# Optimization experiments

Measured on AMD Instinct MI355X. Metric: run time of the kernel, lower is better.

The kernel has to match this reference:

```python
import jax, jax.numpy as jnp
import numpy as np

N = 100000
E = 800000
D_IN = 128
D_HID = 128
D_EMB = 128
D_OUT = 2


def setup_inputs() -> dict:
    key = jax.random.key(0)
    ks = jax.random.split(key, 16)
    x = jax.random.normal(ks[0], (N, D_IN), dtype=jnp.float32)
    edge_index = jax.random.randint(ks[1], (2, E), 0, N, dtype=jnp.int64)

    def lin(k, d_out, d_in, scale):
        return jax.random.normal(k, (d_out, d_in), dtype=jnp.float32) * scale

    s1 = 1.0 / np.sqrt(D_IN)
    s2 = 1.0 / np.sqrt(D_HID)
    s3 = 1.0 / np.sqrt(D_EMB)
    return {
        "x": x,
        "edge_index": edge_index,
        # layer 1: in -> hidden  (lin_l has bias, lin_r no bias, as in PyG SAGEConv)
        "Wl1": lin(ks[2], D_HID, D_IN, s1), "bl1": jnp.zeros((D_HID,), jnp.float32),
        "Wr1": lin(ks[3], D_HID, D_IN, s1),
        # layer 2: hidden -> hidden
        "Wl2": lin(ks[4], D_HID, D_HID, s2), "bl2": jnp.zeros((D_HID,), jnp.float32),
        "Wr2": lin(ks[5], D_HID, D_HID, s2),
        # layer 3: hidden -> embedding
        "Wl3": lin(ks[6], D_EMB, D_HID, s2), "bl3": jnp.zeros((D_EMB,), jnp.float32),
        "Wr3": lin(ks[7], D_EMB, D_HID, s2),
        # output head: embedding -> output (bias)
        "Wo": lin(ks[8], D_OUT, D_EMB, s3), "bo": jnp.zeros((D_OUT,), jnp.float32),
    }


def _sage_conv(x, src, dst, Wl, bl, Wr):
    # mean-aggregate neighbor (source) features onto destination nodes
    msg = x[src]                                             # [E, d]
    agg = jax.ops.segment_sum(msg, dst, num_segments=N)      # [N, d]
    deg = jax.ops.segment_sum(jnp.ones((src.shape[0],), x.dtype), dst, num_segments=N)
    agg = agg / jnp.maximum(deg, 1.0)[:, None]
    # out = lin_l(agg) + lin_r(x)
    return agg @ Wl.T + bl + x @ Wr.T


def reference(x, edge_index, Wl1, bl1, Wr1, Wl2, bl2, Wr2, Wl3, bl3, Wr3, Wo, bo):
    src, dst = edge_index[0], edge_index[1]
    h = jax.nn.relu(_sage_conv(x, src, dst, Wl1, bl1, Wr1))   # dropout is identity in eval
    h = jax.nn.relu(_sage_conv(h, src, dst, Wl2, bl2, Wr2))
    h = _sage_conv(h, src, dst, Wl3, bl3, Wr3)                # no relu on last conv
    return h @ Wo.T + bo                                      # [N, D_OUT]
```

## Files before the change

### kernel.cpp

```cpp
#include <hip/hip_runtime.h>
#include <stdint.h>

typedef unsigned int u32;
typedef unsigned short u16;
typedef __bf16 bf16x8 __attribute__((ext_vector_type(8)));
typedef float floatx16 __attribute__((ext_vector_type(16)));
typedef u32 u32x4 __attribute__((ext_vector_type(4)));
typedef float floatx4 __attribute__((ext_vector_type(4)));

__device__ __forceinline__ u16 f2b(float f) {
    u32 u = __builtin_bit_cast(u32, f);
    u32 r = u + 0x7FFFu + ((u >> 16) & 1u);
    return (u16)(r >> 16);
}
__device__ __forceinline__ float lo2f(u32 u) { return __builtin_bit_cast(float, u << 16); }
__device__ __forceinline__ float hi2f(u32 u) { return __builtin_bit_cast(float, u & 0xFFFF0000u); }

__device__ __forceinline__ void self_detect(const int* ei, const u32* xw, int& is64, int& isbf) {
    int lane = threadIdx.x & 63;
    int v = ei ? ei[2 * lane + 1] : 0;
    unsigned long long b1 = __ballot(v == 0);
    u32 w = xw ? xw[lane] : 0;
    u32 e = (w >> 7) & 0xFF;
    int plaus = (e == 0) || (e >= 90 && e <= 140);
    unsigned long long b2 = __ballot(plaus);
    is64 = (b1 == ~0ULL) ? 1 : 0;
    isbf = (b2 == ~0ULL) ? 1 : 0;
}

__device__ __forceinline__ int load_id(const int* __restrict__ ei, int is64, size_t pos, int N) {
    int v = is64 ? ei[2 * pos] : ei[pos];
    unsigned u = (unsigned)v;
    if (u >= (unsigned)N) u = 0;
    return (int)u;
}

__device__ __forceinline__ float load_f(const void* __restrict__ p, int isbf, size_t i) {
    if (isbf) {
        u16 s = ((const u16*)p)[i];
        return __builtin_bit_cast(float, ((u32)s) << 16);
    }
    return ((const float*)p)[i];
}

#define CH 4096
#define CAPB 3072

__global__ __launch_bounds__(1024) void front_kernel(
    const void* __restrict__ xraw, const int* __restrict__ ei, int E, int N, int cvb,
    u32* __restrict__ xb, int* __restrict__ gcur, u32* __restrict__ csrbkt,
    const void* Wl1, const void* Wr1, const void* Wl2, const void* Wr2,
    const void* Wl3, const void* Wr3, const void* b1, const void* b2,
    const void* b3, const void* Wo, const void* bo,
    u16* __restrict__ Wcp, float* __restrict__ smalls) {
    __shared__ int lhist[1024], loff[1024], lcur[1024], gofs[1024], wsum[16];
    __shared__ u32 ebuf[CH];
    __shared__ u16 ebkt[CH];
    int blk = blockIdx.x;
    int t = threadIdx.x;

    if (blk < cvb) {
        int is64, isbf;
        self_detect(nullptr, (const u32*)xraw, is64, isbf);
        int i = blk * 1024 + t;
        int count4 = N * 16;
        if (i >= count4) return;
        if (isbf) {
            ((u32x4*)xb)[i] = ((const u32x4*)xraw)[i];
        } else {
            const floatx4* f4 = (const floatx4*)xraw;
            floatx4 f0 = f4[2 * i], f1 = f4[2 * i + 1];
            u32x4 o;
            o.x = (u32)f2b(f0.x) | ((u32)f2b(f0.y) << 16);
            o.y = (u32)f2b(f0.z) | ((u32)f2b(f0.w) << 16);
            o.z = (u32)f2b(f1.x) | ((u32)f2b(f1.y) << 16);
            o.w = (u32)f2b(f1.z) | ((u32)f2b(f1.w) << 16);
            ((u32x4*)xb)[i] = o;
        }
        return;
    }
    if (blk < cvb + 12) {
        int is64, isbf;
        self_detect(nullptr, (const u32*)xraw, is64, isbf);
        int tg = (blk - cvb) * 1024 + t;
        int l = tg >> 12;
        int tt = tg & 4095;
        const void* Wl = (l == 0) ? Wl1 : (l == 1) ? Wl2 : Wl3;
        const void* Wr = (l == 0) ? Wr1 : (l == 1) ? Wr2 : Wr3;
        u16* Wout = Wcp + (size_t)l * 32768;
        int lane = tt & 63;
        int jt = (tt >> 6) & 3;
        int s = tt >> 8;
        int n = lane & 31;
        int q = lane >> 5;
        int j = jt * 32 + n;
#pragma unroll
        for (int jj = 0; jj < 8; ++jj) {
            int k = s * 16 + q * 8 + jj;
            float v = (k < 128) ? load_f(Wl, isbf, (size_t)j * 128 + k)
                                : load_f(Wr, isbf, (size_t)j * 128 + (k - 128));
            Wout[tt * 8 + jj] = f2b(v);
        }
        return;
    }
    if (blk == cvb + 12) {
        int is64, isbf;
        self_detect(nullptr, (const u32*)xraw, is64, isbf);
        if (t < 642) {
            float v;
            if (t < 128) v = load_f(b1, isbf, t);
            else if (t < 256) v = load_f(b2, isbf, t - 128);
            else if (t < 384) v = load_f(b3, isbf, t - 256);
            else if (t < 640) v = load_f(Wo, isbf, t - 384);
            else v = load_f(bo, isbf, t - 640);
            smalls[t] = v;
        }
        return;
    }

    int is64, isbf;
    self_detect(ei, nullptr, is64, isbf);
    int cbase = (blk - (cvb + 13)) * CH;
    int cn = E - cbase;
    if (cn > CH) cn = CH;
    lhist[t] = 0;
    __syncthreads();
    int mysrc[4], myb[4], mydl[4];
#pragma unroll
    for (int k = 0; k < 4; ++k) {
        int i = t + k * 1024;
        myb[k] = -1;
        if (i < cn) {
            int e = cbase + i;
            int s, d;
            if (is64) {
                s = (int)((const uint2*)ei)[(size_t)e].x;
                d = (int)((const uint2*)ei)[(size_t)E + e].x;
            } else {
                s = ei[(size_t)e];
                d = ei[(size_t)E + e];
            }
            if ((unsigned)s >= (unsigned)N) s = 0;
            if ((unsigned)d >= (unsigned)N) d = 0;
            mysrc[k] = s;
            mydl[k] = d & 255;
            myb[k] = d >> 8;
            atomicAdd(&lhist[myb[k]], 1);
        }
    }
    __syncthreads();
    int lane = t & 63, wid = t >> 6;
    int v = lhist[t];
    int inc = v;
#pragma unroll
    for (int off = 1; off < 64; off <<= 1) {
        int o = __shfl_up(inc, off);
        if (lane >= off) inc += o;
    }
    if (lane == 63) wsum[wid] = inc;
    __syncthreads();
    int wpre = 0;
    for (int w = 0; w < wid; ++w) wpre += wsum[w];
    int excl = wpre + inc - v;
    loff[t] = excl;
    lcur[t] = excl;
    if (v > 0) gofs[t] = atomicAdd(&gcur[t], v);
    __syncthreads();
#pragma unroll
    for (int k = 0; k < 4; ++k) {
        if (myb[k] >= 0) {
            int pos = atomicAdd(&lcur[myb[k]], 1);
            ebuf[pos] = (u32)mysrc[k] | ((u32)mydl[k] << 24);
            ebkt[pos] = (u16)myb[k];
        }
    }
    __syncthreads();
#pragma unroll
    for (int k = 0; k < 4; ++k) {
        int i = t + k * 1024;
        if (i < cn) {
            int bb = ebkt[i];
            int local = gofs[bb] + (i - loff[bb]);
            if (local < CAPB) csrbkt[(size_t)bb * CAPB + local] = ebuf[i];
        }
    }
}

__global__ __launch_bounds__(512) void csr_build_kernel(
    const u32* __restrict__ csrbkt, const int* __restrict__ gcur,
    int N, int* __restrict__ gtot,
    int* __restrict__ offs, int* __restrict__ cnt,
    int* __restrict__ csr) {
    __shared__ int lh[256], lcur[256], wsum[4];
    __shared__ int sbase;
    __shared__ u32 sbuf[CAPB];
    int t = threadIdx.x;
    int b = blockIdx.x;
    int cb = gcur[b];
    if (cb > CAPB) cb = CAPB;
    const u32* bsrc = csrbkt + (size_t)b * CAPB;
    int d0 = b << 8;
    if (t < 256) lh[t] = 0;
    __syncthreads();
    for (int i = t; i < cb; i += 512) atomicAdd(&lh[bsrc[i] >> 24], 1);
    __syncthreads();
    int lane = t & 63, wid = t >> 6;
    if (t < 256) {
        int v = lh[t];
        int inc = v;
#pragma unroll
        for (int off = 1; off < 64; off <<= 1) {
            int o = __shfl_up(inc, off);
            if (lane >= off) inc += o;
        }
        if (lane == 63) wsum[wid] = inc;
    }
    __syncthreads();
    if (t < 256) {
        int v = lh[t];
        int inc = v;
#pragma unroll
        for (int off = 1; off < 64; off <<= 1) {
            int o = __shfl_up(inc, off);
            if (lane >= off) inc += o;
        }
        int wpre = 0;
        for (int w = 0; w < wid; ++w) wpre += wsum[w];
        int excl = wpre + inc - v;
        lcur[t] = excl;
        int d = d0 + t;
        if (d < N) {
            lh[t] = excl;
            cnt[d] = v;
        }
    }
    if (t == 0) sbase = atomicAdd(gtot, cb);
    __syncthreads();
    int base = sbase;
    if (t < 256) {
        int d = d0 + t;
        if (d < N) offs[d] = base + lh[t];
    }
    for (int i = t; i < cb; i += 512) {
        u32 e = bsrc[i];
        int pos = atomicAdd(&lcur[e >> 24], 1);
        sbuf[pos] = e & 0xFFFFFFu;
    }
    __syncthreads();
    for (int i = t; i < cb; i += 512) csr[base + i] = (int)sbuf[i];
}


__global__ void agg_kernel(const u32* __restrict__ F2, const int* __restrict__ offs,
                           const int* __restrict__ cnt, const int* __restrict__ csr,
                           u32* __restrict__ Aout, int N, int tstride) {
    int sub = blockIdx.x / tstride;
    int tile = blockIdx.x % tstride;
    int w = threadIdx.x >> 6;
    int lane = threadIdx.x & 63;
    int nd0 = tile * 128 + sub * 16 + w * 4;
    if (nd0 >= N) return;
    int nd1 = nd0 + 4 < N ? nd0 + 4 : N;
    for (int nd = nd0; nd < nd1; ++nd) {
        int start = offs[nd];
        int num = cnt[nd];
        float a0 = 0.f, a1 = 0.f;
        int i = 0;
        for (; i + 8 <= num; i += 8) {
            int s0 = csr[start + i + 0], s1 = csr[start + i + 1];
            int s2 = csr[start + i + 2], s3 = csr[start + i + 3];
            int s4 = csr[start + i + 4], s5 = csr[start + i + 5];
            int s6 = csr[start + i + 6], s7 = csr[start + i + 7];
            u32 u0 = F2[(size_t)s0 * 64 + lane];
            u32 u1 = F2[(size_t)s1 * 64 + lane];
            u32 u2 = F2[(size_t)s2 * 64 + lane];
            u32 u3 = F2[(size_t)s3 * 64 + lane];
            u32 u4 = F2[(size_t)s4 * 64 + lane];
            u32 u5 = F2[(size_t)s5 * 64 + lane];
            u32 u6 = F2[(size_t)s6 * 64 + lane];
            u32 u7 = F2[(size_t)s7 * 64 + lane];
            a0 += lo2f(u0) + lo2f(u1) + lo2f(u2) + lo2f(u3) +
                  lo2f(u4) + lo2f(u5) + lo2f(u6) + lo2f(u7);
            a1 += hi2f(u0) + hi2f(u1) + hi2f(u2) + hi2f(u3) +
                  hi2f(u4) + hi2f(u5) + hi2f(u6) + hi2f(u7);
        }
        for (; i + 4 <= num; i += 4) {
            int s0 = csr[start + i + 0], s1 = csr[start + i + 1];
            int s2 = csr[start + i + 2], s3 = csr[start + i + 3];
            u32 u0 = F2[(size_t)s0 * 64 + lane];
            u32 u1 = F2[(size_t)s1 * 64 + lane];
            u32 u2 = F2[(size_t)s2 * 64 + lane];
            u32 u3 = F2[(size_t)s3 * 64 + lane];
            a0 += lo2f(u0) + lo2f(u1) + lo2f(u2) + lo2f(u3);
            a1 += hi2f(u0) + hi2f(u1) + hi2f(u2) + hi2f(u3);
        }
        for (; i < num; ++i) {
            u32 u = F2[(size_t)csr[start + i] * 64 + lane];
            a0 += lo2f(u);
            a1 += hi2f(u);
        }
        float sc = 1.0f / (float)(num > 1 ? num : 1);
        a0 *= sc;
        a1 *= sc;
        Aout[(size_t)nd * 64 + lane] = (u32)f2b(a0) | ((u32)f2b(a1) << 16);
    }
}

__global__ __launch_bounds__(256, 4) void gemm_kernel(
    const u32* __restrict__ aggb, u32* Fio,
    const u16* __restrict__ Wcp, const float* __restrict__ biasf,
    int N, int relu, const float* __restrict__ headw,
    const u32* __restrict__ xw, void* __restrict__ outp) {
    __shared__ u16 ldsT[4][32][68];
    int tid = threadIdx.x;
    int w = tid >> 6;
    int lane = tid & 63;
    int nbase = blockIdx.x * 128;
    int n = lane & 31;
    int q = lane >> 5;
    int rowl = w * 32 + n;
    int node = nbase + rowl;
    int nodeC = (node < N) ? node : (N - 1);
    const u32* aRow = aggb + (size_t)nodeC * 64 + q * 4;
    const u32* fRow = Fio + (size_t)nodeC * 64 + q * 4;

    floatx16 acc0 = 0.0f, acc1 = 0.0f, acc2 = 0.0f, acc3 = 0.0f;

#pragma unroll
    for (int s = 0; s < 16; ++s) {
        const u32* ap = (s < 8) ? (aRow + (size_t)s * 8) : (fRow + (size_t)(s - 8) * 8);
        bf16x8 a = *reinterpret_cast<const bf16x8*>(ap);
        const u16* bp = Wcp + (size_t)((s * 4) * 64 + lane) * 8;
        bf16x8 b0 = *reinterpret_cast<const bf16x8*>(bp);
        bf16x8 b1 = *reinterpret_cast<const bf16x8*>(bp + 64 * 8);
        bf16x8 b2 = *reinterpret_cast<const bf16x8*>(bp + 2 * 64 * 8);
        bf16x8 b3 = *reinterpret_cast<const bf16x8*>(bp + 3 * 64 * 8);
        acc0 = __builtin_amdgcn_mfma_f32_32x32x16_bf16(a, b0, acc0, 0, 0, 0);
        acc1 = __builtin_amdgcn_mfma_f32_32x32x16_bf16(a, b1, acc1, 0, 0, 0);
        acc2 = __builtin_amdgcn_mfma_f32_32x32x16_bf16(a, b2, acc2, 0, 0, 0);
        acc3 = __builtin_amdgcn_mfma_f32_32x32x16_bf16(a, b3, acc3, 0, 0, 0);
    }

    int mbase = nbase + w * 32;
    floatx16 accs[4] = {acc0, acc1, acc2, acc3};

    if (outp == nullptr) {
        int rowg = mbase + n;
        int okrow = rowg < N;
#pragma unroll
        for (int h = 0; h < 2; ++h) {
#pragma unroll
            for (int jt2 = 0; jt2 < 2; ++jt2) {
                int jt = h * 2 + jt2;
                int j0 = jt * 32 + n;
                float bf = biasf[j0];
#pragma unroll
                for (int r = 0; r < 16; ++r) {
                    int row = (r & 3) + 8 * (r >> 2) + 4 * q;
                    float v = accs[jt][r] + bf;
                    if (relu) v = fmaxf(v, 0.0f);
                    ldsT[w][row][jt2 * 32 + n] = f2b(v);
                }
            }
#pragma unroll
            for (int i = 0; i < 4; ++i) {
                const u16* lp = &ldsT[w][n][q * 8 + i * 16];
                uint2 lo = *reinterpret_cast<const uint2*>(lp);
                uint2 hi = *reinterpret_cast<const uint2*>(lp + 4);
                if (okrow) {
                    u32x4 o;
                    o.x = lo.x; o.y = lo.y; o.z = hi.x; o.w = hi.y;
                    *reinterpret_cast<u32x4*>(&Fio[(size_t)rowg * 64 + h * 32 + q * 4 + i * 8]) = o;
                }
            }
        }
    } else {
        int is64, isbf;
        self_detect(nullptr, xw, is64, isbf);
#pragma unroll
        for (int r = 0; r < 16; ++r) {
            float p0 = 0.f, p1 = 0.f;
#pragma unroll
            for (int jt = 0; jt < 4; ++jt) {
                int j = jt * 32 + n;
                float v = accs[jt][r] + biasf[j];
                p0 += v * headw[j];
                p1 += v * headw[128 + j];
            }
#pragma unroll
            for (int off = 16; off > 0; off >>= 1) {
                p0 += __shfl_xor(p0, off);
                p1 += __shfl_xor(p1, off);
            }
            if (n == 0) {
                int row = (r & 3) + 8 * (r >> 2) + 4 * q;
                int nodeS = mbase + row;
                if (nodeS < N) {
                    float o0 = p0 + headw[256];
                    float o1 = p1 + headw[257];
                    if (isbf)
                        ((u32*)outp)[nodeS] = (u32)f2b(o0) | ((u32)f2b(o1) << 16);
                    else
                        ((float2*)outp)[nodeS] = make_float2(o0, o1);
                }
            }
        }
    }
}

extern "C" void kernel_launch(void* const* d_in, const int* in_sizes, int n_in,
                              void* d_out, int out_size, void* d_ws, size_t ws_size,
                              hipStream_t stream) {
    const int N = in_sizes[0] / 128;
    const int E = in_sizes[1] / 2;

    const void* x = d_in[0];
    const int* ei = (const int*)d_in[1];
    const void* Wl[3] = {d_in[2], d_in[5], d_in[8]};
    const void* bl[3] = {d_in[3], d_in[6], d_in[9]};
    const void* Wr[3] = {d_in[4], d_in[7], d_in[10]};
    const void* Wo = d_in[11];
    const void* bo = d_in[12];

    char* p = (char*)d_ws;
    auto alloc = [&](size_t bytes) -> char* {
        char* r = p;
        p += (bytes + 255) & ~(size_t)255;
        return r;
    };
    int* offs = (int*)alloc((size_t)N * 4);
    int* cnt = (int*)alloc((size_t)N * 4);
    float* smalls = (float*)alloc(642 * 4);
    int* gcur = (int*)alloc(1025 * 4);
    int* csr = (int*)alloc(((size_t)E + CAPB + 64) * 4);
    u16* Wcp = (u16*)alloc((size_t)3 * 4096 * 8 * 2);
    u32* xb = (u32*)alloc((size_t)(N + 1) * 64 * 4);
    u32* aggb = (u32*)alloc((size_t)N * 64 * 4);
    u32* csrbkt = aggb;
    int* gtot = gcur + 1024;
    (void)ws_size;

    const int NB = (N + 255) / 256;
    const int cvb = (N * 16 + 1023) / 1024;
    const int sb = (E + CH - 1) / CH;
    const int gb = (N + 127) / 128;
    const int tstride = (gb + 7) & ~7;
    const int ab = 8 * tstride;

    hipMemsetAsync(gcur, 0, 1025 * 4, stream);
    front_kernel<<<cvb + 13 + sb, 1024, 0, stream>>>(
        x, ei, E, N, cvb, xb, gcur, csrbkt,
        Wl[0], Wr[0], Wl[1], Wr[1], Wl[2], Wr[2],
        bl[0], bl[1], bl[2], Wo, bo, Wcp, smalls);
    csr_build_kernel<<<NB, 512, 0, stream>>>(csrbkt, gcur, N, gtot, offs, cnt, csr);

    agg_kernel<<<ab, 256, 0, stream>>>(xb, offs, cnt, csr, aggb, N, tstride);
    gemm_kernel<<<gb, 256, 0, stream>>>(aggb, xb, Wcp, smalls, N, 1, nullptr, nullptr, nullptr);
    agg_kernel<<<ab, 256, 0, stream>>>(xb, offs, cnt, csr, aggb, N, tstride);
    gemm_kernel<<<gb, 256, 0, stream>>>(aggb, xb, Wcp + 32768, smalls + 128, N, 1, nullptr, nullptr, nullptr);
    agg_kernel<<<ab, 256, 0, stream>>>(xb, offs, cnt, csr, aggb, N, tstride);
    gemm_kernel<<<gb, 256, 0, stream>>>(aggb, xb, Wcp + 65536, smalls + 256, N, 0,
                                        smalls + 384, (const u32*)x, d_out);
}
```

Baseline: 330.3 us.

## Switch GEMM to 16x16x32 MFMA with 64-node blocks and repacked weights

Repacks the concatenated weights for the 16x16x32 bf16 MFMA layout and rewrites the GEMM so each wave computes 16 nodes by 128 outputs. Each block now covers 64 nodes, which doubles the grid. This cuts accumulator registers per wave and adds more blocks, so the memory-bound GEMM should get more parallelism and latency hiding. In exchange it issues more B-fragment loads per node and needs a new LDS transpose and head-reduction path.

```diff
diff --git a/kernel.cpp b/kernel.cpp
--- a/kernel.cpp
+++ b/kernel.cpp
@@ -4,9 +4,15 @@
 typedef unsigned int u32;
 typedef unsigned short u16;
 typedef __bf16 bf16x8 __attribute__((ext_vector_type(8)));
+typedef float floatx4 __attribute__((ext_vector_type(4)));
+typedef u32 u32x4 __attribute__((ext_vector_type(4)));
+typedef float floatx4f __attribute__((ext_vector_type(4)));
+typedef float floatx4v __attribute__((ext_vector_type(4)));
 typedef float floatx16 __attribute__((ext_vector_type(16)));
-typedef u32 u32x4 __attribute__((ext_vector_type(4)));
-typedef float floatx4 __attribute__((ext_vector_type(4)));
+typedef float floatx4b __attribute__((ext_vector_type(4)));
+typedef float floatx4c __attribute__((ext_vector_type(4)));
+typedef float floatx4d __attribute__((ext_vector_type(4)));
+typedef float floatx4e __attribute__((ext_vector_type(4)));
 
 __device__ __forceinline__ u16 f2b(float f) {
     u32 u = __builtin_bit_cast(u32, f);
@@ -26,13 +32,6 @@
     unsigned long long b2 = __ballot(plaus);
     is64 = (b1 == ~0ULL) ? 1 : 0;
     isbf = (b2 == ~0ULL) ? 1 : 0;
-}
-
-__device__ __forceinline__ int load_id(const int* __restrict__ ei, int is64, size_t pos, int N) {
-    int v = is64 ? ei[2 * pos] : ei[pos];
-    unsigned u = (unsigned)v;
-    if (u >= (unsigned)N) u = 0;
-    return (int)u;
 }
 
 __device__ __forceinline__ float load_f(const void* __restrict__ p, int isbf, size_t i) {
@@ -68,8 +67,9 @@
         if (isbf) {
             ((u32x4*)xb)[i] = ((const u32x4*)xraw)[i];
         } else {
-            const floatx4* f4 = (const floatx4*)xraw;
-            floatx4 f0 = f4[2 * i], f1 = f4[2 * i + 1];
+            typedef float fx4 __attribute__((ext_vector_type(4)));
+            const fx4* f4 = (const fx4*)xraw;
+            fx4 f0 = f4[2 * i], f1 = f4[2 * i + 1];
             u32x4 o;
             o.x = (u32)f2b(f0.x) | ((u32)f2b(f0.y) << 16);
             o.y = (u32)f2b(f0.z) | ((u32)f2b(f0.w) << 16);
@@ -88,15 +88,15 @@
         const void* Wl = (l == 0) ? Wl1 : (l == 1) ? Wl2 : Wl3;
         const void* Wr = (l == 0) ? Wr1 : (l == 1) ? Wr2 : Wr3;
         u16* Wout = Wcp + (size_t)l * 32768;
-        int lane = tt & 63;
-        int jt = (tt >> 6) & 3;
-        int s = tt >> 8;
-        int n = lane & 31;
-        int q = lane >> 5;
-        int j = jt * 32 + n;
+        int ln = tt & 63;
+        int c = tt >> 6;
+        int sk = c >> 3;
+        int jt = c & 7;
+        int j = jt * 16 + (ln & 15);
+        int kb = sk * 32 + (ln >> 4) * 8;
 #pragma unroll
         for (int jj = 0; jj < 8; ++jj) {
-            int k = s * 16 + q * 8 + jj;
+            int k = kb + jj;
             float v = (k < 128) ? load_f(Wl, isbf, (size_t)j * 128 + k)
                                 : load_f(Wr, isbf, (size_t)j * 128 + (k - 128));
             Wout[tt * 8 + jj] = f2b(v);
@@ -310,91 +310,84 @@
     const u32* __restrict__ aggb, u32* Fio,
     const u16* __restrict__ Wcp, const float* __restrict__ biasf,
     int N, int relu, const float* __restrict__ headw,
-    const u32* __restrict__ xw, void* __restrict__ outp) {
-    __shared__ u16 ldsT[4][32][68];
+    const u32* __restrict__ xw, void* __restrict__ outp, int gstride) {
+    __shared__ u16 ldsT[4][16][132];
     int tid = threadIdx.x;
     int w = tid >> 6;
     int lane = tid & 63;
-    int nbase = blockIdx.x * 128;
-    int n = lane & 31;
-    int q = lane >> 5;
-    int rowl = w * 32 + n;
-    int node = nbase + rowl;
+    int r16 = lane & 15;
+    int g4 = lane >> 4;
+    int tile = blockIdx.x % gstride;
+    int half = blockIdx.x / gstride;
+    int nbase = tile * 128 + half * 64;
+    if (nbase >= N) return;
+    int nd0 = nbase + w * 16;
+    int node = nd0 + r16;
     int nodeC = (node < N) ? node : (N - 1);
-    const u32* aRow = aggb + (size_t)nodeC * 64 + q * 4;
-    const u32* fRow = Fio + (size_t)nodeC * 64 + q * 4;
-
-    floatx16 acc0 = 0.0f, acc1 = 0.0f, acc2 = 0.0f, acc3 = 0.0f;
-
-#pragma unroll
-    for (int s = 0; s < 16; ++s) {
-        const u32* ap = (s < 8) ? (aRow + (size_t)s * 8) : (fRow + (size_t)(s - 8) * 8);
+    const u32* aRow = aggb + (size_t)nodeC * 64 + g4 * 4;
+    const u32* fRow = Fio + (size_t)nodeC * 64 + g4 * 4;
+
+    floatx4 acc[8];
+#pragma unroll
+    for (int jt = 0; jt < 8; ++jt) acc[jt] = 0.0f;
+
+#pragma unroll
+    for (int s = 0; s < 8; ++s) {
+        const u32* ap = (s < 4) ? (aRow + (size_t)s * 16) : (fRow + (size_t)(s - 4) * 16);
         bf16x8 a = *reinterpret_cast<const bf16x8*>(ap);
-        const u16* bp = Wcp + (size_t)((s * 4) * 64 + lane) * 8;
-        bf16x8 b0 = *reinterpret_cast<const bf16x8*>(bp);
-        bf16x8 b1 = *reinterpret_cast<const bf16x8*>(bp + 64 * 8);
-        bf16x8 b2 = *reinterpret_cast<const bf16x8*>(bp + 2 * 64 * 8);
-        bf16x8 b3 = *reinterpret_cast<const bf16x8*>(bp + 3 * 64 * 8);
-        acc0 = __builtin_amdgcn_mfma_f32_32x32x16_bf16(a, b0, acc0, 0, 0, 0);
-        acc1 = __builtin_amdgcn_mfma_f32_32x32x16_bf16(a, b1, acc1, 0, 0, 0);
-        acc2 = __builtin_amdgcn_mfma_f32_32x32x16_bf16(a, b2, acc2, 0, 0, 0);
-        acc3 = __builtin_amdgcn_mfma_f32_32x32x16_bf16(a, b3, acc3, 0, 0, 0);
-    }
-
-    int mbase = nbase + w * 32;
-    floatx16 accs[4] = {acc0, acc1, acc2, acc3};
+        const u16* bp = Wcp + (size_t)((s * 8) * 64 + lane) * 8;
+#pragma unroll
+        for (int jt = 0; jt < 8; ++jt) {
+            bf16x8 b = *reinterpret_cast<const bf16x8*>(bp + (size_t)jt * 64 * 8);
+            acc[jt] = __builtin_amdgcn_mfma_f32_16x16x32_bf16(a, b, acc[jt], 0, 0, 0);
+        }
+    }
 
     if (outp == nullptr) {
-        int rowg = mbase + n;
-        int okrow = rowg < N;
-#pragma unroll
-        for (int h = 0; h < 2; ++h) {
-#pragma unroll
-            for (int jt2 = 0; jt2 < 2; ++jt2) {
-                int jt = h * 2 + jt2;
-                int j0 = jt * 32 + n;
-                float bf = biasf[j0];
-#pragma unroll
-                for (int r = 0; r < 16; ++r) {
-                    int row = (r & 3) + 8 * (r >> 2) + 4 * q;
-                    float v = accs[jt][r] + bf;
-                    if (relu) v = fmaxf(v, 0.0f);
-                    ldsT[w][row][jt2 * 32 + n] = f2b(v);
-                }
-            }
+#pragma unroll
+        for (int jt = 0; jt < 8; ++jt) {
+            int j = jt * 16 + r16;
+            float bf = biasf[j];
+#pragma unroll
+            for (int r = 0; r < 4; ++r) {
+                float v = acc[jt][r] + bf;
+                if (relu) v = fmaxf(v, 0.0f);
+                ldsT[w][g4 * 4 + r][j] = f2b(v);
+            }
+        }
+        int rowg = nd0 + r16;
+        if (rowg < N) {
+            u32* drow = &Fio[(size_t)rowg * 64 + g4 * 16];
 #pragma unroll
             for (int i = 0; i < 4; ++i) {
-                const u16* lp = &ldsT[w][n][q * 8 + i * 16];
+                const u16* lp = &ldsT[w][r16][g4 * 32 + i * 8];
                 uint2 lo = *reinterpret_cast<const uint2*>(lp);
                 uint2 hi = *reinterpret_cast<const uint2*>(lp + 4);
-                if (okrow) {
-                    u32x4 o;
-                    o.x = lo.x; o.y = lo.y; o.z = hi.x; o.w = hi.y;
-                    *reinterpret_cast<u32x4*>(&Fio[(size_t)rowg * 64 + h * 32 + q * 4 + i * 8]) = o;
-                }
+                u32x4 o;
+                o.x = lo.x; o.y = lo.y; o.z = hi.x; o.w = hi.y;
+                *reinterpret_cast<u32x4*>(drow + i * 4) = o;
             }
         }
     } else {
         int is64, isbf;
         self_detect(nullptr, xw, is64, isbf);
 #pragma unroll
-        for (int r = 0; r < 16; ++r) {
+        for (int r = 0; r < 4; ++r) {
             float p0 = 0.f, p1 = 0.f;
 #pragma unroll
-            for (int jt = 0; jt < 4; ++jt) {
-                int j = jt * 32 + n;
-                float v = accs[jt][r] + biasf[j];
+            for (int jt = 0; jt < 8; ++jt) {
+                int j = jt * 16 + r16;
+                float v = acc[jt][r] + biasf[j];
                 p0 += v * headw[j];
                 p1 += v * headw[128 + j];
             }
 #pragma unroll
-            for (int off = 16; off > 0; off >>= 1) {
+            for (int off = 8; off > 0; off >>= 1) {
                 p0 += __shfl_xor(p0, off);
                 p1 += __shfl_xor(p1, off);
             }
-            if (n == 0) {
-                int row = (r & 3) + 8 * (r >> 2) + 4 * q;
-                int nodeS = mbase + row;
+            if (r16 == 0) {
+                int nodeS = nd0 + g4 * 4 + r;
                 if (nodeS < N) {
                     float o0 = p0 + headw[256];
                     float o1 = p1 + headw[257];
@@ -446,6 +439,8 @@
     const int gb = (N + 127) / 128;
     const int tstride = (gb + 7) & ~7;
     const int ab = 8 * tstride;
+    const int gstride = tstride;
+    const int ggrid = 2 * gstride;
 
     hipMemsetAsync(gcur, 0, 1025 * 4, stream);
     front_kernel<<<cvb + 13 + sb, 1024, 0, stream>>>(
@@ -455,10 +450,10 @@
     csr_build_kernel<<<NB, 512, 0, stream>>>(csrbkt, gcur, N, gtot, offs, cnt, csr);
 
     agg_kernel<<<ab, 256, 0, stream>>>(xb, offs, cnt, csr, aggb, N, tstride);
-    gemm_kernel<<<gb, 256, 0, stream>>>(aggb, xb, Wcp, smalls, N, 1, nullptr, nullptr, nullptr);
+    gemm_kernel<<<ggrid, 256, 0, stream>>>(aggb, xb, Wcp, smalls, N, 1, nullptr, nullptr, nullptr, gstride);
     agg_kernel<<<ab, 256, 0, stream>>>(xb, offs, cnt, csr, aggb, N, tstride);
-    gemm_kernel<<<gb, 256, 0, stream>>>(aggb, xb, Wcp + 32768, smalls + 128, N, 1, nullptr, nullptr, nullptr);
+    gemm_kernel<<<ggrid, 256, 0, stream>>>(aggb, xb, Wcp + 32768, smalls + 128, N, 1, nullptr, nullptr, nullptr, gstride);
     agg_kernel<<<ab, 256, 0, stream>>>(xb, offs, cnt, csr, aggb, N, tstride);
-    gemm_kernel<<<gb, 256, 0, stream>>>(aggb, xb, Wcp + 65536, smalls + 256, N, 0,
-                                        smalls + 384, (const u32*)x, d_out);
-}
+    gemm_kernel<<<ggrid, 256, 0, stream>>>(aggb, xb, Wcp + 65536, smalls + 256, N, 0,
+                                           smalls + 384, (const u32*)x, d_out, gstride);
+}
```

Result: slower. 342.4 us (+3.7%).
